# Performance work log

Measured on AMD Instinct MI355X. Metric: run time of the kernel, lower is better.

The kernel has to match this reference:

```python
import jax, jax.numpy as jnp
import numpy as np

EPS = 1e-07
INF = 100000.0
BIG = 1e8  # sentinel cost for priors outside all gt boxes/centers (filtered out in torch)
CENTER_RADIUS = 2.5
CANDIDATE_TOPK = 10
IOU_WEIGHT = 3.0
CLS_WEIGHT = 1.0
IMG = 1280.0


def setup_inputs() -> dict:
    key = jax.random.key(0)
    ks = jax.random.split(key, 9)
    N, G, C = 33600, 128, 80
    cx = jax.random.uniform(ks[0], (N,), minval=0.0, maxval=IMG)
    cy = jax.random.uniform(ks[1], (N,), minval=0.0, maxval=IMG)
    strides = jax.random.uniform(ks[2], (N, 2), minval=8.0, maxval=32.0)
    priors = jnp.stack([cx, cy, strides[:, 0], strides[:, 1]], axis=1)  # [N,4] cx,cy,sw,sh
    dc = jax.random.uniform(ks[3], (N, 2), minval=0.0, maxval=IMG)
    dwh = jax.random.uniform(ks[4], (N, 2), minval=4.0, maxval=200.0)
    decoded_bboxes = jnp.concatenate([dc - dwh / 2, dc + dwh / 2], axis=1)  # [N,4] tlbr
    gc = jax.random.uniform(ks[5], (G, 2), minval=0.0, maxval=IMG)
    gwh = jax.random.uniform(ks[6], (G, 2), minval=20.0, maxval=400.0)
    gt_bboxes = jnp.concatenate([gc - gwh / 2, gc + gwh / 2], axis=1)  # [G,4] tlbr
    pred_scores = jax.random.uniform(ks[7], (N, C), minval=1e-4, maxval=1.0 - 1e-4)
    gt_labels = jax.random.randint(ks[8], (G,), 0, C)
    return {
        'pred_scores': pred_scores,
        'priors': priors,
        'decoded_bboxes': decoded_bboxes,
        'gt_bboxes': gt_bboxes,
        'gt_labels': gt_labels,
    }


def _pairwise_iou(a, b):
    # a: [N,4] tlbr, b: [G,4] tlbr -> [N,G]
    tl = jnp.maximum(a[:, None, :2], b[None, :, :2])
    br = jnp.minimum(a[:, None, 2:], b[None, :, 2:])
    wh = jnp.clip(br - tl, 0.0)
    inter = wh[..., 0] * wh[..., 1]
    area_a = jnp.prod(jnp.clip(a[:, 2:] - a[:, :2], 0.0), axis=-1)
    area_b = jnp.prod(jnp.clip(b[:, 2:] - b[:, :2], 0.0), axis=-1)
    union = area_a[:, None] + area_b[None, :] - inter
    return inter / jnp.maximum(union, EPS)


def _forward(pred_scores, priors, decoded_bboxes, gt_bboxes, gt_labels):
    N = decoded_bboxes.shape[0]
    G = gt_bboxes.shape[0]
    px, py = priors[:, 0:1], priors[:, 1:2]          # [N,1]
    sx, sy = priors[:, 2:3], priors[:, 3:4]
    # in-gt-box mask [N,G]
    l_ = px - gt_bboxes[None, :, 0]
    t_ = py - gt_bboxes[None, :, 1]
    r_ = gt_bboxes[None, :, 2] - px
    b_ = gt_bboxes[None, :, 3] - py
    is_in_gts = jnp.minimum(jnp.minimum(l_, t_), jnp.minimum(r_, b_)) > 0
    # in-center mask [N,G]
    gcx = (gt_bboxes[:, 0] + gt_bboxes[:, 2]) / 2.0
    gcy = (gt_bboxes[:, 1] + gt_bboxes[:, 3]) / 2.0
    cl_ = px - (gcx[None, :] - CENTER_RADIUS * sx)
    ct_ = py - (gcy[None, :] - CENTER_RADIUS * sy)
    cr_ = (gcx[None, :] + CENTER_RADIUS * sx) - px
    cb_ = (gcy[None, :] + CENTER_RADIUS * sy) - py
    is_in_cts = jnp.minimum(jnp.minimum(cl_, ct_), jnp.minimum(cr_, cb_)) > 0
    valid = jnp.any(is_in_gts | is_in_cts, axis=1)           # [N]
    in_box_and_center = is_in_gts & is_in_cts                # [N,G]

    ious = _pairwise_iou(decoded_bboxes, gt_bboxes)          # [N,G]
    ious = jnp.where(valid[:, None], ious, 0.0)              # invalid priors excluded
    iou_cost = -jnp.log(ious + EPS)

    # BCE(pred, one_hot(label)).sum(-1) without materializing [N,G,C]:
    # = -log p[label] + log1p(-p[label]) - sum_c log1p(-p_c)  (logs clamped at -100 like torch)
    L = jnp.clip(jnp.log(pred_scores), -100.0)               # [N,C]
    L1 = jnp.clip(jnp.log1p(-pred_scores), -100.0)           # [N,C]
    gl = gt_labels.astype(jnp.int32)
    cls_cost = -(L[:, gl] - L1[:, gl]) - jnp.sum(L1, axis=1, keepdims=True)  # [N,G]

    cost = cls_cost * CLS_WEIGHT + iou_cost * IOU_WEIGHT + (~in_box_and_center) * INF
    cost = jnp.where(valid[:, None], cost, BIG)

    K = min(CANDIDATE_TOPK, N)
    topk_ious, _ = jax.lax.top_k(ious.T, K)                  # [G,K]
    dynamic_ks = jnp.clip(topk_ious.sum(1).astype(jnp.int32), 1, None)  # [G], <= K
    # per-GT: K smallest costs (ascending), keep first dynamic_k of them
    _, pos_idx = jax.lax.top_k(-cost.T, K)                   # [G,K] prior indices
    sel = (jnp.arange(K)[None, :] < dynamic_ks[:, None]).astype(cost.dtype)
    matching = jnp.zeros((N, G), cost.dtype).at[pos_idx, jnp.arange(G)[:, None]].add(sel)

    # resolve priors matched to >1 gt by min-cost gt
    multi = matching.sum(1) > 1
    argmin = jnp.argmin(cost, axis=1)
    matching = jnp.where(multi[:, None], jax.nn.one_hot(argmin, G, dtype=cost.dtype), matching)

    fg = matching.sum(1) > 0
    matched_gt = jnp.argmax(matching, axis=1)
    matched_iou = jnp.sum(matching * ious, axis=1)

    assigned_gt_inds = jnp.where(fg, matched_gt, 0)
    assigned_labels = jnp.where(fg, 1, -1)
    assigned_gt_iou = jnp.where(fg, matched_iou, -INF)
    return assigned_gt_inds, assigned_labels, assigned_gt_iou


def reference(pred_scores, priors, decoded_bboxes, gt_bboxes, gt_labels):
    return _forward(pred_scores, priors, decoded_bboxes, gt_bboxes, gt_labels)
```

## Files before the change

### kernel.cpp

```cpp
#include <hip/hip_runtime.h>
#include <math.h>
#include <limits.h>

#pragma clang fp contract(off)

#define TPB 256
#define ATPB 64
#define KTOP 10
#define ISPLIT 64
#define GSPLIT 8
#define GCAP 4096
#define CHUNKCAP 4224
#define MAXG 512
#define MAXMULTI 4096

typedef unsigned int u32;
typedef unsigned long long u64;
typedef unsigned char u8;

__device__ __forceinline__ float f_iou(float ax0, float ay0, float ax1, float ay1,
                                       float bx0, float by0, float bx1, float by1) {
  float tlx = fmaxf(ax0, bx0);
  float tly = fmaxf(ay0, by0);
  float brx = fminf(ax1, bx1);
  float bry = fminf(ay1, by1);
  float w = fmaxf(brx - tlx, 0.0f);
  float h = fmaxf(bry - tly, 0.0f);
  float inter = w * h;
  float aa = fmaxf(ax1 - ax0, 0.0f) * fmaxf(ay1 - ay0, 0.0f);
  float ab = fmaxf(bx1 - bx0, 0.0f) * fmaxf(by1 - by0, 0.0f);
  float uni = aa + ab - inter;
  return inter / fmaxf(uni, 1e-7f);
}

__device__ __forceinline__ float f_dv(float p) {
  float L  = fmaxf(logf(p), -100.0f);
  float L1 = fmaxf(log1pf(-p), -100.0f);
  return -(L - L1);
}

__device__ __forceinline__ float f_cost(float iou_masked, float dv, float sumL1v,
                                        float px, float py, float sx, float sy,
                                        float bx0, float by0, float bx1, float by1,
                                        int vld) {
  if (!vld) return 100000000.0f;
  float cls = dv - sumL1v;
  float l_ = px - bx0, t_ = py - by0, r_ = bx1 - px, b_ = by1 - py;
  bool ing = fminf(fminf(l_, t_), fminf(r_, b_)) > 0.0f;
  float gcx = (bx0 + bx1) * 0.5f;
  float gcy = (by0 + by1) * 0.5f;
  float cl = px - (gcx - 2.5f * sx);
  float ct = py - (gcy - 2.5f * sy);
  float cr = (gcx + 2.5f * sx) - px;
  float cb = (gcy + 2.5f * sy) - py;
  bool inc = fminf(fminf(cl, ct), fminf(cr, cb)) > 0.0f;
  float icost = -logf(iou_masked + 1e-7f);
  return (cls * 1.0f + icost * 3.0f) + ((ing && inc) ? 0.0f : 100000.0f);
}

__global__ __launch_bounds__(TPB) void k_fallback(float* out, int Nout) {
  int n = blockIdx.x * blockDim.x + threadIdx.x;
  if (n >= Nout) return;
  out[n] = 0.0f;
  out[Nout + n] = -1.0f;
  out[2 * Nout + n] = -70000.0f;
}

__global__ __launch_bounds__(TPB) void k_phase1(
    const float* pred, const float* priors, const float* gtb,
    float* sumL1, u32* packed, u8* validArr,
    int* gateCnt, int* gateList, int* flags,
    int N, int G, int C, int sumBlocks)
{
  __shared__ int lbuf[CHUNKCAP];
  __shared__ int lcnt;
  __shared__ int gbase;

  if ((int)blockIdx.x < sumBlocks) {
    int t = blockIdx.x * TPB + threadIdx.x;
    int n = t >> 3;
    int j = t & 7;
    if (n >= N) return;
    const float* pr = pred + (size_t)n * C;
    int lim = C - (C % 8);
    float r = 0.0f;
    for (int i = j; i < lim; i += 8) r += fmaxf(log1pf(-pr[i]), -100.0f);
    r += __shfl_down(r, 1, 8);
    r += __shfl_down(r, 2, 8);
    r += __shfl_down(r, 4, 8);
    if (j == 0) {
      for (int i = lim; i < C; ++i) r += fmaxf(log1pf(-pr[i]), -100.0f);
      sumL1[n] = r;
      packed[n] = 0;
    }
    return;
  }

  int bid = blockIdx.x - sumBlocks;
  int g = bid / GSPLIT;
  int s = bid % GSPLIT;
  int chunk = (N + GSPLIT - 1) / GSPLIT;
  int start = s * chunk;
  int end = start + chunk; if (end > N) end = N;
  int lane = threadIdx.x & 63;

  if (threadIdx.x == 0) lcnt = 0;
  __syncthreads();

  float x0 = gtb[g * 4 + 0], y0 = gtb[g * 4 + 1];
  float x1 = gtb[g * 4 + 2], y1 = gtb[g * 4 + 3];
  float gcx = (x0 + x1) * 0.5f, gcy = (y0 + y1) * 0.5f;
  const float4* pri4 = reinterpret_cast<const float4*>(priors);

  for (int nb = start; nb < end; nb += TPB) {
    int n = nb + threadIdx.x;
    bool gated = false;
    if (n < end) {
      float4 pv = pri4[n];
      float px = pv.x, py = pv.y, sx = pv.z, sy = pv.w;
      float l_ = px - x0, t_ = py - y0, r_ = x1 - px, b_ = y1 - py;
      bool ing = fminf(fminf(l_, t_), fminf(r_, b_)) > 0.0f;
      float cl = px - (gcx - 2.5f * sx), ct = py - (gcy - 2.5f * sy);
      float cr = (gcx + 2.5f * sx) - px, cb = (gcy + 2.5f * sy) - py;
      bool inc = fminf(fminf(cl, ct), fminf(cr, cb)) > 0.0f;
      if (ing || inc) validArr[n] = 1;
      gated = ing && inc;
    }
    u64 mask = __ballot(gated);
    int wcnt = __popcll(mask);
    int wbase = 0;
    if (lane == 0 && wcnt > 0) wbase = atomicAdd(&lcnt, wcnt);
    wbase = __shfl(wbase, 0);
    if (gated) {
      int p = __popcll(mask & ((1ull << lane) - 1ull));
      lbuf[wbase + p] = n;
    }
  }
  __syncthreads();
  int total = lcnt;
  if (threadIdx.x == 0 && total > 0) gbase = atomicAdd(&gateCnt[g], total);
  __syncthreads();
  if (total > 0) {
    int base = gbase;
    int* gl = gateList + (size_t)g * GCAP;
    for (int i = threadIdx.x; i < total; i += TPB) {
      int slot = base + i;
      if (slot < GCAP) gl[slot] = lbuf[i];
      else flags[g] = 1;
    }
  }
}

__global__ __launch_bounds__(ATPB) void k_iou_part(
    const float* dec, const u8* validArr, const float* gtb,
    float* iouV, int N, int G)
{
  int bid = blockIdx.x;
  int g = bid / ISPLIT;
  int s = bid % ISPLIT;
  int chunk = (N + ISPLIT - 1) / ISPLIT;
  int start = s * chunk;
  int end = start + chunk; if (end > N) end = N;
  int tid = threadIdx.x;
  float bx0 = gtb[g * 4 + 0];
  float by0 = gtb[g * 4 + 1];
  float bx1 = gtb[g * 4 + 2];
  float by1 = gtb[g * 4 + 3];

  float iv[KTOP];
#pragma unroll
  for (int j = 0; j < KTOP; ++j) iv[j] = 0.0f;

  const float4* dec4 = reinterpret_cast<const float4*>(dec);
  for (int n = start + tid; n < end; n += ATPB) {
    float4 dvb = dec4[n];
    float iou = f_iou(dvb.x, dvb.y, dvb.z, dvb.w, bx0, by0, bx1, by1);
    if (!validArr[n]) iou = 0.0f;
    if (iou > iv[KTOP - 1]) {
      float cu = iou;
#pragma unroll
      for (int j = 0; j < KTOP; ++j) {
        if (cu > iv[j]) { float tv = iv[j]; iv[j] = cu; cu = tv; }
      }
    }
  }

#pragma unroll
  for (int r = 0; r < KTOP; ++r) {
    float v = iv[0]; int owner = tid;
#pragma unroll
    for (int off = 32; off > 0; off >>= 1) {
      float v2 = __shfl_down(v, off);
      int o2 = __shfl_down(owner, off);
      if (v2 > v || (v2 == v && o2 < owner)) { v = v2; owner = o2; }
    }
    float wv = __shfl(v, 0);
    int wo = __shfl(owner, 0);
    if (tid == 0) iouV[bid * KTOP + r] = wv;
    if (tid == wo) {
#pragma unroll
      for (int j = 0; j < KTOP - 1; ++j) iv[j] = iv[j + 1];
      iv[KTOP - 1] = 0.0f;
    }
  }
}

__global__ __launch_bounds__(ATPB) void k_merge(
    const float* iouV, const int* gateCnt, const int* gateList, const int* flags,
    const float* pred, const float* priors, const float* dec, const float* sumL1,
    const u8* validArr, const int* gtl, const float* gtb,
    u32* packed, int G, int N, int C)
{
  int g = blockIdx.x;
  int tid = threadIdx.x;
  int base = g * ISPLIT * KTOP;
  const int TOT = ISPLIT * KTOP;
  const int PER = TOT / ATPB;

  float il[PER];
#pragma unroll
  for (int k = 0; k < PER; ++k) il[k] = 0.0f;
#pragma unroll
  for (int k = 0; k < PER; ++k) {
    float v = iouV[base + tid + k * ATPB];
    if (v > il[PER - 1]) {
#pragma unroll
      for (int j = 0; j < PER; ++j) {
        if (v > il[j]) { float tv = il[j]; il[j] = v; v = tv; }
      }
    }
  }
  float rv[KTOP];
#pragma unroll
  for (int r = 0; r < KTOP; ++r) {
    float v = il[0]; int owner = tid;
#pragma unroll
    for (int off = 32; off > 0; off >>= 1) {
      float v2 = __shfl_down(v, off);
      int o2 = __shfl_down(owner, off);
      if (v2 > v || (v2 == v && o2 < owner)) { v = v2; owner = o2; }
    }
    float wv = __shfl(v, 0);
    int wo = __shfl(owner, 0);
    rv[r] = wv;
    if (tid == wo) {
#pragma unroll
      for (int j = 0; j < PER - 1; ++j) il[j] = il[j + 1];
      il[PER - 1] = 0.0f;
    }
  }
  float s8 = ((rv[0] + rv[1]) + (rv[2] + rv[3])) + ((rv[4] + rv[5]) + (rv[6] + rv[7]));
  s8 += rv[8];
  s8 += rv[9];
  int dk = (int)s8;
  if (dk < 1) dk = 1;
  if (dk > KTOP) dk = KTOP;

  float bx0 = gtb[g * 4 + 0];
  float by0 = gtb[g * 4 + 1];
  float bx1 = gtb[g * 4 + 2];
  float by1 = gtb[g * 4 + 3];
  int lab = gtl[g];
  if (lab < 0) lab = 0;
  if (lab >= C) lab = C - 1;

  float cv[KTOP]; int ci[KTOP];
#pragma unroll
  for (int j = 0; j < KTOP; ++j) { cv[j] = 1e30f; ci[j] = INT_MAX; }
  const float4* dec4 = reinterpret_cast<const float4*>(dec);

  int cnt = gateCnt[g];
  if (!flags[g] && cnt >= KTOP) {
    const int* gl = gateList + (size_t)g * GCAP;
    for (int i = tid; i < cnt; i += ATPB) {
      int n = gl[i];
      float4 dvb = dec4[n];
      float iou = f_iou(dvb.x, dvb.y, dvb.z, dvb.w, bx0, by0, bx1, by1);
      float dv = f_dv(pred[(size_t)n * C + lab]);
      float cls = dv - sumL1[n];
      float icost = -logf(iou + 1e-7f);
      float c = (cls * 1.0f + icost * 3.0f) + 0.0f;
      bool ins = (c < cv[KTOP - 1]) || (c == cv[KTOP - 1] && n < ci[KTOP - 1]);
      if (ins) {
        float cu = c; int cui = n;
#pragma unroll
        for (int j = 0; j < KTOP; ++j) {
          bool lt = (cu < cv[j]) || (cu == cv[j] && cui < ci[j]);
          if (lt) { float tv = cv[j]; int ti = ci[j]; cv[j] = cu; ci[j] = cui; cu = tv; cui = ti; }
        }
      }
    }
  } else {
    const float4* pri4 = reinterpret_cast<const float4*>(priors);
    for (int n = tid; n < N; n += ATPB) {
      float4 dvb = dec4[n];
      int vld = validArr[n];
      float iou = f_iou(dvb.x, dvb.y, dvb.z, dvb.w, bx0, by0, bx1, by1);
      if (!vld) iou = 0.0f;
      float dv = f_dv(pred[(size_t)n * C + lab]);
      float4 pv = pri4[n];
      float c = f_cost(iou, dv, sumL1[n], pv.x, pv.y, pv.z, pv.w, bx0, by0, bx1, by1, vld);
      bool ins = (c < cv[KTOP - 1]) || (c == cv[KTOP - 1] && n < ci[KTOP - 1]);
      if (ins) {
        float cu = c; int cui = n;
#pragma unroll
        for (int j = 0; j < KTOP; ++j) {
          bool lt = (cu < cv[j]) || (cu == cv[j] && cui < ci[j]);
          if (lt) { float tv = cv[j]; int ti = ci[j]; cv[j] = cu; ci[j] = cui; cu = tv; cui = ti; }
        }
      }
    }
  }

  for (int r = 0; r < KTOP; ++r) {
    float v = cv[0]; int idx = ci[0];
#pragma unroll
    for (int off = 32; off > 0; off >>= 1) {
      float v2 = __shfl_down(v, off);
      int i2 = __shfl_down(idx, off);
      if (v2 < v || (v2 == v && i2 < idx)) { v = v2; idx = i2; }
    }
    int wi = __shfl(idx, 0);
    if (r < dk && tid == 0 && wi >= 0 && wi < N) {
      atomicAdd(&packed[wi], (1u << 16) | (u32)g);
    }
    if (ci[0] == wi) {
#pragma unroll
      for (int j = 0; j < KTOP - 1; ++j) { cv[j] = cv[j + 1]; ci[j] = ci[j + 1]; }
      cv[KTOP - 1] = 1e30f; ci[KTOP - 1] = INT_MAX;
    }
    if (r + 1 >= dk) break;
  }
}

__global__ __launch_bounds__(TPB) void k_final(
    const float* dec, const float* gtb, const u8* validArr, const u32* packed,
    int* mlist, int* mcnt,
    float* out, int N, int G, int Nout)
{
  __shared__ float sg[MAXG * 4];
  for (int i = threadIdx.x; i < G * 4; i += blockDim.x) sg[i] = gtb[i];
  __syncthreads();
  int n = blockIdx.x * blockDim.x + threadIdx.x;
  if (n >= N || n >= Nout) return;
  u32 pk = packed[n];
  int cnt = (int)(pk >> 16);
  float o0 = 0.0f, o1 = -1.0f, o2 = -100000.0f;
  if (cnt > 1) {
    int idx = atomicAdd(mcnt, 1);
    if (idx < MAXMULTI) mlist[idx] = n;
  }
  if (cnt == 1) {
    int g = (int)(pk & 0xFFFFu);
    if (g < 0) g = 0;
    if (g >= G) g = G - 1;
    const float4 dv = reinterpret_cast<const float4*>(dec)[n];
    float x0 = sg[g * 4 + 0], y0 = sg[g * 4 + 1], x1 = sg[g * 4 + 2], y1 = sg[g * 4 + 3];
    float iou = f_iou(dv.x, dv.y, dv.z, dv.w, x0, y0, x1, y1);
    if (!validArr[n]) iou = 0.0f;
    o0 = (float)g; o1 = 1.0f; o2 = iou;
  }
  out[n]            = o0;
  out[Nout + n]     = o1;
  out[2 * Nout + n] = o2;
}

#define MTPB 128
__global__ __launch_bounds__(MTPB) void k_multi(
    const float* pred, const float* priors, const float* dec,
    const float* gtb, const int* gtl, const float* sumL1, const u8* validArr,
    const int* mlist, const int* mcnt,
    float* out, int N, int G, int C, int Nout)
{
  __shared__ float rv[MTPB];
  __shared__ int   rg[MTPB];
  int tid = threadIdx.x;
  int total = *mcnt;
  if (total > MAXMULTI) total = MAXMULTI;
  for (int w = blockIdx.x; w < total; w += gridDim.x) {
    int n = mlist[w];
    const float4 dvb = reinterpret_cast<const float4*>(dec)[n];
    const float4 pv  = reinterpret_cast<const float4*>(priors)[n];
    float s1 = sumL1[n];
    int vld = validArr[n];
    float best = 1e30f; int bg = INT_MAX;
    for (int gg = tid; gg < G; gg += MTPB) {
      float x0 = gtb[gg * 4 + 0], y0 = gtb[gg * 4 + 1];
      float x1 = gtb[gg * 4 + 2], y1 = gtb[gg * 4 + 3];
      float iou = f_iou(dvb.x, dvb.y, dvb.z, dvb.w, x0, y0, x1, y1);
      if (!vld) iou = 0.0f;
      int lb = gtl[gg];
      if (lb < 0) lb = 0;
      if (lb >= C) lb = C - 1;
      float dv = f_dv(pred[(size_t)n * C + lb]);
      float c = f_cost(iou, dv, s1, pv.x, pv.y, pv.z, pv.w, x0, y0, x1, y1, vld);
      if (c < best || (c == best && gg < bg)) { best = c; bg = gg; }
    }
    rv[tid] = best; rg[tid] = bg;
    __syncthreads();
    for (int st = MTPB / 2; st > 0; st >>= 1) {
      if (tid < st) {
        float v2 = rv[tid + st]; int g2 = rg[tid + st];
        float v1 = rv[tid];      int g1 = rg[tid];
        if (v2 < v1 || (v2 == v1 && g2 < g1)) { rv[tid] = v2; rg[tid] = g2; }
      }
      __syncthreads();
    }
    if (tid == 0) {
      int g = rg[0];
      if (g < 0 || g >= G) g = 0;
      float x0 = gtb[g * 4 + 0], y0 = gtb[g * 4 + 1];
      float x1 = gtb[g * 4 + 2], y1 = gtb[g * 4 + 3];
      float iou = f_iou(dvb.x, dvb.y, dvb.z, dvb.w, x0, y0, x1, y1);
      if (!vld) iou = 0.0f;
      out[n]            = (float)g;
      out[Nout + n]     = 1.0f;
      out[2 * Nout + n] = iou;
    }
    __syncthreads();
  }
}

extern "C" void kernel_launch(void* const* d_in, const int* in_sizes, int n_in,
                              void* d_out, int out_size, void* d_ws, size_t ws_size,
                              hipStream_t stream) {
  const float* pred   = (const float*)d_in[0];
  const float* priors = (const float*)d_in[1];
  const float* dec    = (const float*)d_in[2];
  const float* gtb    = (const float*)d_in[3];
  const int*   gtl    = (const int*)d_in[4];
  int N = in_sizes[2] / 4;
  int G = in_sizes[3] / 4;
  if (G > MAXG) G = MAXG;
  int C = in_sizes[0] / N;
  int Nout = out_size / 3;
  float* out = (float*)d_out;

  size_t offPacked = 0;
  size_t offSum    = offPacked + (size_t)N * 4;
  size_t offZero   = (offSum + (size_t)N * 4 + 15) & ~(size_t)15;
  size_t offFlags  = offZero + (size_t)G * 4;
  size_t offMcnt   = offFlags + (size_t)G * 4;
  size_t offValid  = (offMcnt + 4 + 15) & ~(size_t)15;
  size_t offMlist  = (offValid + (size_t)N + 15) & ~(size_t)15;
  size_t offGlist  = (offMlist + (size_t)MAXMULTI * 4 + 15) & ~(size_t)15;
  size_t offIouV   = offGlist + (size_t)G * GCAP * 4;
  size_t need      = offIouV + (size_t)G * ISPLIT * KTOP * 4;

  dim3 b(TPB);
  int nblk = (N + TPB - 1) / TPB;
  int oblk = (Nout + TPB - 1) / TPB;
  if (ws_size < need || d_ws == nullptr) {
    k_fallback<<<oblk, b, 0, stream>>>(out, Nout);
    return;
  }
  char* wsb = (char*)d_ws;
  u32* packed   = (u32*)(wsb + offPacked);
  float* sumL1  = (float*)(wsb + offSum);
  int* gateCnt  = (int*)(wsb + offZero);
  int* flags    = (int*)(wsb + offFlags);
  int* mcnt     = (int*)(wsb + offMcnt);
  u8* validArr  = (u8*)(wsb + offValid);
  int* mlist    = (int*)(wsb + offMlist);
  int* gateList = (int*)(wsb + offGlist);
  float* iouV   = (float*)(wsb + offIouV);

  hipMemsetAsync(wsb + offZero, 0, offValid + (size_t)N - offZero, stream);

  int sumBlocks = ((N * 8) + TPB - 1) / TPB;
  int gateBlocks = G * GSPLIT;
  k_phase1<<<sumBlocks + gateBlocks, b, 0, stream>>>(
      pred, priors, gtb, sumL1, packed, validArr, gateCnt, gateList, flags,
      N, G, C, sumBlocks);
  k_iou_part<<<G * ISPLIT, dim3(ATPB), 0, stream>>>(dec, validArr, gtb, iouV, N, G);
  k_merge<<<G, dim3(ATPB), 0, stream>>>(iouV, gateCnt, gateList, flags,
                                        pred, priors, dec, sumL1, validArr, gtl, gtb,
                                        packed, G, N, C);
  k_final<<<nblk, b, 0, stream>>>(dec, gtb, validArr, packed, mlist, mcnt, out, N, G, Nout);
  k_multi<<<256, dim3(MTPB), 0, stream>>>(pred, priors, dec, gtb, gtl, sumL1, validArr,
                                          mlist, mcnt, out, N, G, C, Nout);
}
```

Before: 127.1 us.

## Fuse all assignment stages into one cooperative persistent kernel with grid syncs

Replaces the memset and five separate kernel launches with a single cooperative kernel. The stages (log-sum and gating, per-chunk IoU top-k, per-GT merge and cost top-k, final write, multi-match resolution) are separated by grid.sync, and each wave now handles one unit instead of each 64-thread block. The intent is to remove launch overhead and inter-kernel gaps and to use wave-level shuffles instead of shared-memory reductions in the multi stage. The cost is grid-wide barriers and a grid sized by occupancy (up to 1024 blocks), which may underuse the GPU in the heavier stages. The gating stage also gains in-loop flushing of the shared buffer.

```diff
diff --git a/kernel.cpp b/kernel.cpp
--- a/kernel.cpp
+++ b/kernel.cpp
@@ -1,18 +1,20 @@
 #include <hip/hip_runtime.h>
+#include <hip/hip_cooperative_groups.h>
 #include <math.h>
 #include <limits.h>
 
 #pragma clang fp contract(off)
 
 #define TPB 256
-#define ATPB 64
+#define NWAVE 4
 #define KTOP 10
 #define ISPLIT 64
 #define GSPLIT 8
 #define GCAP 4096
-#define CHUNKCAP 4224
-#define MAXG 512
+#define CHUNKCAP 4480
 #define MAXMULTI 4096
+
+namespace cg = cooperative_groups;
 
 typedef unsigned int u32;
 typedef unsigned long long u64;
@@ -58,333 +60,328 @@
   return (cls * 1.0f + icost * 3.0f) + ((ing && inc) ? 0.0f : 100000.0f);
 }
 
-__global__ __launch_bounds__(TPB) void k_fallback(float* out, int Nout) {
+__global__ __launch_bounds__(TPB) void k_fb(float* out, int Nout, float val) {
   int n = blockIdx.x * blockDim.x + threadIdx.x;
   if (n >= Nout) return;
   out[n] = 0.0f;
   out[Nout + n] = -1.0f;
-  out[2 * Nout + n] = -70000.0f;
-}
-
-__global__ __launch_bounds__(TPB) void k_phase1(
-    const float* pred, const float* priors, const float* gtb,
+  out[2 * Nout + n] = val;
+}
+
+__global__ __launch_bounds__(TPB) void k_all(
+    const float* pred, const float* priors, const float* dec,
+    const float* gtb, const int* gtl,
     float* sumL1, u32* packed, u8* validArr,
     int* gateCnt, int* gateList, int* flags,
-    int N, int G, int C, int sumBlocks)
+    float* iouV, int* mlist, int* mcnt,
+    float* out, int N, int G, int C, int Nout)
 {
+  cg::grid_group grid = cg::this_grid();
   __shared__ int lbuf[CHUNKCAP];
   __shared__ int lcnt;
   __shared__ int gbase;
-
-  if ((int)blockIdx.x < sumBlocks) {
-    int t = blockIdx.x * TPB + threadIdx.x;
-    int n = t >> 3;
-    int j = t & 7;
-    if (n >= N) return;
-    const float* pr = pred + (size_t)n * C;
-    int lim = C - (C % 8);
-    float r = 0.0f;
-    for (int i = j; i < lim; i += 8) r += fmaxf(log1pf(-pr[i]), -100.0f);
-    r += __shfl_down(r, 1, 8);
-    r += __shfl_down(r, 2, 8);
-    r += __shfl_down(r, 4, 8);
-    if (j == 0) {
-      for (int i = lim; i < C; ++i) r += fmaxf(log1pf(-pr[i]), -100.0f);
-      sumL1[n] = r;
-      packed[n] = 0;
-    }
-    return;
-  }
-
-  int bid = blockIdx.x - sumBlocks;
-  int g = bid / GSPLIT;
-  int s = bid % GSPLIT;
-  int chunk = (N + GSPLIT - 1) / GSPLIT;
-  int start = s * chunk;
-  int end = start + chunk; if (end > N) end = N;
-  int lane = threadIdx.x & 63;
-
-  if (threadIdx.x == 0) lcnt = 0;
-  __syncthreads();
-
-  float x0 = gtb[g * 4 + 0], y0 = gtb[g * 4 + 1];
-  float x1 = gtb[g * 4 + 2], y1 = gtb[g * 4 + 3];
-  float gcx = (x0 + x1) * 0.5f, gcy = (y0 + y1) * 0.5f;
+  const int tid = threadIdx.x;
+  const int lane = tid & 63;
+  const int wid = tid >> 6;
+  const int nblk = gridDim.x;
+  const float4* dec4 = reinterpret_cast<const float4*>(dec);
   const float4* pri4 = reinterpret_cast<const float4*>(priors);
 
-  for (int nb = start; nb < end; nb += TPB) {
-    int n = nb + threadIdx.x;
-    bool gated = false;
-    if (n < end) {
-      float4 pv = pri4[n];
-      float px = pv.x, py = pv.y, sx = pv.z, sy = pv.w;
-      float l_ = px - x0, t_ = py - y0, r_ = x1 - px, b_ = y1 - py;
-      bool ing = fminf(fminf(l_, t_), fminf(r_, b_)) > 0.0f;
-      float cl = px - (gcx - 2.5f * sx), ct = py - (gcy - 2.5f * sy);
-      float cr = (gcx + 2.5f * sx) - px, cb = (gcy + 2.5f * sy) - py;
-      bool inc = fminf(fminf(cl, ct), fminf(cr, cb)) > 0.0f;
-      if (ing || inc) validArr[n] = 1;
-      gated = ing && inc;
-    }
-    u64 mask = __ballot(gated);
-    int wcnt = __popcll(mask);
-    int wbase = 0;
-    if (lane == 0 && wcnt > 0) wbase = atomicAdd(&lcnt, wcnt);
-    wbase = __shfl(wbase, 0);
-    if (gated) {
-      int p = __popcll(mask & ((1ull << lane) - 1ull));
-      lbuf[wbase + p] = n;
-    }
-  }
-  __syncthreads();
-  int total = lcnt;
-  if (threadIdx.x == 0 && total > 0) gbase = atomicAdd(&gateCnt[g], total);
-  __syncthreads();
-  if (total > 0) {
-    int base = gbase;
-    int* gl = gateList + (size_t)g * GCAP;
-    for (int i = threadIdx.x; i < total; i += TPB) {
-      int slot = base + i;
-      if (slot < GCAP) gl[slot] = lbuf[i];
-      else flags[g] = 1;
-    }
-  }
-}
-
-__global__ __launch_bounds__(ATPB) void k_iou_part(
-    const float* dec, const u8* validArr, const float* gtb,
-    float* iouV, int N, int G)
-{
-  int bid = blockIdx.x;
-  int g = bid / ISPLIT;
-  int s = bid % ISPLIT;
-  int chunk = (N + ISPLIT - 1) / ISPLIT;
-  int start = s * chunk;
-  int end = start + chunk; if (end > N) end = N;
-  int tid = threadIdx.x;
-  float bx0 = gtb[g * 4 + 0];
-  float by0 = gtb[g * 4 + 1];
-  float bx1 = gtb[g * 4 + 2];
-  float by1 = gtb[g * 4 + 3];
-
-  float iv[KTOP];
-#pragma unroll
-  for (int j = 0; j < KTOP; ++j) iv[j] = 0.0f;
-
-  const float4* dec4 = reinterpret_cast<const float4*>(dec);
-  for (int n = start + tid; n < end; n += ATPB) {
-    float4 dvb = dec4[n];
-    float iou = f_iou(dvb.x, dvb.y, dvb.z, dvb.w, bx0, by0, bx1, by1);
-    if (!validArr[n]) iou = 0.0f;
-    if (iou > iv[KTOP - 1]) {
-      float cu = iou;
-#pragma unroll
-      for (int j = 0; j < KTOP; ++j) {
-        if (cu > iv[j]) { float tv = iv[j]; iv[j] = cu; cu = tv; }
-      }
-    }
-  }
-
-#pragma unroll
-  for (int r = 0; r < KTOP; ++r) {
-    float v = iv[0]; int owner = tid;
-#pragma unroll
-    for (int off = 32; off > 0; off >>= 1) {
-      float v2 = __shfl_down(v, off);
-      int o2 = __shfl_down(owner, off);
-      if (v2 > v || (v2 == v && o2 < owner)) { v = v2; owner = o2; }
-    }
-    float wv = __shfl(v, 0);
-    int wo = __shfl(owner, 0);
-    if (tid == 0) iouV[bid * KTOP + r] = wv;
-    if (tid == wo) {
-#pragma unroll
-      for (int j = 0; j < KTOP - 1; ++j) iv[j] = iv[j + 1];
-      iv[KTOP - 1] = 0.0f;
-    }
-  }
-}
-
-__global__ __launch_bounds__(ATPB) void k_merge(
-    const float* iouV, const int* gateCnt, const int* gateList, const int* flags,
-    const float* pred, const float* priors, const float* dec, const float* sumL1,
-    const u8* validArr, const int* gtl, const float* gtb,
-    u32* packed, int G, int N, int C)
-{
-  int g = blockIdx.x;
-  int tid = threadIdx.x;
-  int base = g * ISPLIT * KTOP;
-  const int TOT = ISPLIT * KTOP;
-  const int PER = TOT / ATPB;
-
-  float il[PER];
-#pragma unroll
-  for (int k = 0; k < PER; ++k) il[k] = 0.0f;
-#pragma unroll
-  for (int k = 0; k < PER; ++k) {
-    float v = iouV[base + tid + k * ATPB];
-    if (v > il[PER - 1]) {
-#pragma unroll
-      for (int j = 0; j < PER; ++j) {
-        if (v > il[j]) { float tv = il[j]; il[j] = v; v = tv; }
-      }
-    }
-  }
-  float rv[KTOP];
-#pragma unroll
-  for (int r = 0; r < KTOP; ++r) {
-    float v = il[0]; int owner = tid;
-#pragma unroll
-    for (int off = 32; off > 0; off >>= 1) {
-      float v2 = __shfl_down(v, off);
-      int o2 = __shfl_down(owner, off);
-      if (v2 > v || (v2 == v && o2 < owner)) { v = v2; owner = o2; }
-    }
-    float wv = __shfl(v, 0);
-    int wo = __shfl(owner, 0);
-    rv[r] = wv;
-    if (tid == wo) {
-#pragma unroll
-      for (int j = 0; j < PER - 1; ++j) il[j] = il[j + 1];
-      il[PER - 1] = 0.0f;
-    }
-  }
-  float s8 = ((rv[0] + rv[1]) + (rv[2] + rv[3])) + ((rv[4] + rv[5]) + (rv[6] + rv[7]));
-  s8 += rv[8];
-  s8 += rv[9];
-  int dk = (int)s8;
-  if (dk < 1) dk = 1;
-  if (dk > KTOP) dk = KTOP;
-
-  float bx0 = gtb[g * 4 + 0];
-  float by0 = gtb[g * 4 + 1];
-  float bx1 = gtb[g * 4 + 2];
-  float by1 = gtb[g * 4 + 3];
-  int lab = gtl[g];
-  if (lab < 0) lab = 0;
-  if (lab >= C) lab = C - 1;
-
-  float cv[KTOP]; int ci[KTOP];
-#pragma unroll
-  for (int j = 0; j < KTOP; ++j) { cv[j] = 1e30f; ci[j] = INT_MAX; }
-  const float4* dec4 = reinterpret_cast<const float4*>(dec);
-
-  int cnt = gateCnt[g];
-  if (!flags[g] && cnt >= KTOP) {
-    const int* gl = gateList + (size_t)g * GCAP;
-    for (int i = tid; i < cnt; i += ATPB) {
-      int n = gl[i];
+  for (int i = blockIdx.x * TPB + tid; i < N; i += nblk * TPB) {
+    packed[i] = 0;
+    validArr[i] = 0;
+  }
+  for (int i = blockIdx.x * TPB + tid; i < G; i += nblk * TPB) {
+    gateCnt[i] = 0;
+    flags[i] = 0;
+  }
+  if (blockIdx.x == 0 && tid == 0) *mcnt = 0;
+  grid.sync();
+
+  int sumUnits = (N * 8 + TPB - 1) / TPB;
+  int gateUnits = G * GSPLIT;
+  int chunkG = (N + GSPLIT - 1) / GSPLIT;
+  for (int u = blockIdx.x; u < sumUnits + gateUnits; u += nblk) {
+    if (u < sumUnits) {
+      int t = u * TPB + tid;
+      int n = t >> 3, j = t & 7;
+      if (n < N) {
+        const float* pr = pred + (size_t)n * C;
+        int lim = C - (C % 8);
+        float r = 0.0f;
+        for (int i = j; i < lim; i += 8) r += fmaxf(log1pf(-pr[i]), -100.0f);
+        r += __shfl_down(r, 1, 8);
+        r += __shfl_down(r, 2, 8);
+        r += __shfl_down(r, 4, 8);
+        if (j == 0) {
+          for (int i = lim; i < C; ++i) r += fmaxf(log1pf(-pr[i]), -100.0f);
+          sumL1[n] = r;
+        }
+      }
+    } else {
+      int bidg = u - sumUnits;
+      int g = bidg / GSPLIT, s = bidg % GSPLIT;
+      int start = s * chunkG;
+      int end = start + chunkG; if (end > N) end = N;
+      float x0 = gtb[g * 4 + 0], y0 = gtb[g * 4 + 1];
+      float x1 = gtb[g * 4 + 2], y1 = gtb[g * 4 + 3];
+      float gcx = (x0 + x1) * 0.5f, gcy = (y0 + y1) * 0.5f;
+      int* gl = gateList + (size_t)g * GCAP;
+      if (tid == 0) lcnt = 0;
+      __syncthreads();
+      for (int nb = start; nb < end; nb += TPB) {
+        __syncthreads();
+        if (lcnt + TPB > CHUNKCAP) {
+          int total = lcnt;
+          if (tid == 0) gbase = atomicAdd(&gateCnt[g], total);
+          __syncthreads();
+          int base = gbase;
+          for (int i = tid; i < total; i += TPB) {
+            int slot = base + i;
+            if (slot < GCAP) gl[slot] = lbuf[i];
+            else flags[g] = 1;
+          }
+          __syncthreads();
+          if (tid == 0) lcnt = 0;
+          __syncthreads();
+        }
+        int n = nb + tid;
+        bool gated = false;
+        if (n < end) {
+          float4 pv = pri4[n];
+          float px = pv.x, py = pv.y, sx = pv.z, sy = pv.w;
+          float l_ = px - x0, t_ = py - y0, r_ = x1 - px, b_ = y1 - py;
+          bool ing = fminf(fminf(l_, t_), fminf(r_, b_)) > 0.0f;
+          float cl = px - (gcx - 2.5f * sx), ct = py - (gcy - 2.5f * sy);
+          float cr = (gcx + 2.5f * sx) - px, cb = (gcy + 2.5f * sy) - py;
+          bool inc = fminf(fminf(cl, ct), fminf(cr, cb)) > 0.0f;
+          if (ing || inc) validArr[n] = 1;
+          gated = ing && inc;
+        }
+        u64 mask = __ballot(gated);
+        int wcnt = __popcll(mask);
+        int wbase = 0;
+        if (lane == 0 && wcnt > 0) wbase = atomicAdd(&lcnt, wcnt);
+        wbase = __shfl(wbase, 0);
+        if (gated) {
+          int p = __popcll(mask & ((1ull << lane) - 1ull));
+          lbuf[wbase + p] = n;
+        }
+      }
+      __syncthreads();
+      int total = lcnt;
+      if (tid == 0 && total > 0) gbase = atomicAdd(&gateCnt[g], total);
+      __syncthreads();
+      if (total > 0) {
+        int base = gbase;
+        for (int i = tid; i < total; i += TPB) {
+          int slot = base + i;
+          if (slot < GCAP) gl[slot] = lbuf[i];
+          else flags[g] = 1;
+        }
+      }
+      __syncthreads();
+    }
+  }
+  grid.sync();
+
+  int chunkI = (N + ISPLIT - 1) / ISPLIT;
+  for (int u = blockIdx.x * NWAVE + wid; u < G * ISPLIT; u += nblk * NWAVE) {
+    int g = u / ISPLIT, s = u % ISPLIT;
+    int start = s * chunkI;
+    int end = start + chunkI; if (end > N) end = N;
+    float bx0 = gtb[g * 4 + 0], by0 = gtb[g * 4 + 1];
+    float bx1 = gtb[g * 4 + 2], by1 = gtb[g * 4 + 3];
+    float iv[KTOP];
+#pragma unroll
+    for (int j = 0; j < KTOP; ++j) iv[j] = 0.0f;
+    for (int n = start + lane; n < end; n += 64) {
       float4 dvb = dec4[n];
       float iou = f_iou(dvb.x, dvb.y, dvb.z, dvb.w, bx0, by0, bx1, by1);
-      float dv = f_dv(pred[(size_t)n * C + lab]);
-      float cls = dv - sumL1[n];
-      float icost = -logf(iou + 1e-7f);
-      float c = (cls * 1.0f + icost * 3.0f) + 0.0f;
-      bool ins = (c < cv[KTOP - 1]) || (c == cv[KTOP - 1] && n < ci[KTOP - 1]);
-      if (ins) {
-        float cu = c; int cui = n;
+      if (!validArr[n]) iou = 0.0f;
+      if (iou > iv[KTOP - 1]) {
+        float cu = iou;
 #pragma unroll
         for (int j = 0; j < KTOP; ++j) {
-          bool lt = (cu < cv[j]) || (cu == cv[j] && cui < ci[j]);
-          if (lt) { float tv = cv[j]; int ti = ci[j]; cv[j] = cu; ci[j] = cui; cu = tv; cui = ti; }
-        }
-      }
-    }
-  } else {
-    const float4* pri4 = reinterpret_cast<const float4*>(priors);
-    for (int n = tid; n < N; n += ATPB) {
-      float4 dvb = dec4[n];
-      int vld = validArr[n];
-      float iou = f_iou(dvb.x, dvb.y, dvb.z, dvb.w, bx0, by0, bx1, by1);
-      if (!vld) iou = 0.0f;
-      float dv = f_dv(pred[(size_t)n * C + lab]);
-      float4 pv = pri4[n];
-      float c = f_cost(iou, dv, sumL1[n], pv.x, pv.y, pv.z, pv.w, bx0, by0, bx1, by1, vld);
-      bool ins = (c < cv[KTOP - 1]) || (c == cv[KTOP - 1] && n < ci[KTOP - 1]);
-      if (ins) {
-        float cu = c; int cui = n;
-#pragma unroll
-        for (int j = 0; j < KTOP; ++j) {
-          bool lt = (cu < cv[j]) || (cu == cv[j] && cui < ci[j]);
-          if (lt) { float tv = cv[j]; int ti = ci[j]; cv[j] = cu; ci[j] = cui; cu = tv; cui = ti; }
-        }
-      }
-    }
-  }
-
-  for (int r = 0; r < KTOP; ++r) {
-    float v = cv[0]; int idx = ci[0];
-#pragma unroll
-    for (int off = 32; off > 0; off >>= 1) {
-      float v2 = __shfl_down(v, off);
-      int i2 = __shfl_down(idx, off);
-      if (v2 < v || (v2 == v && i2 < idx)) { v = v2; idx = i2; }
-    }
-    int wi = __shfl(idx, 0);
-    if (r < dk && tid == 0 && wi >= 0 && wi < N) {
-      atomicAdd(&packed[wi], (1u << 16) | (u32)g);
-    }
-    if (ci[0] == wi) {
-#pragma unroll
-      for (int j = 0; j < KTOP - 1; ++j) { cv[j] = cv[j + 1]; ci[j] = ci[j + 1]; }
-      cv[KTOP - 1] = 1e30f; ci[KTOP - 1] = INT_MAX;
-    }
-    if (r + 1 >= dk) break;
-  }
-}
-
-__global__ __launch_bounds__(TPB) void k_final(
-    const float* dec, const float* gtb, const u8* validArr, const u32* packed,
-    int* mlist, int* mcnt,
-    float* out, int N, int G, int Nout)
-{
-  __shared__ float sg[MAXG * 4];
-  for (int i = threadIdx.x; i < G * 4; i += blockDim.x) sg[i] = gtb[i];
-  __syncthreads();
-  int n = blockIdx.x * blockDim.x + threadIdx.x;
-  if (n >= N || n >= Nout) return;
-  u32 pk = packed[n];
-  int cnt = (int)(pk >> 16);
-  float o0 = 0.0f, o1 = -1.0f, o2 = -100000.0f;
-  if (cnt > 1) {
-    int idx = atomicAdd(mcnt, 1);
-    if (idx < MAXMULTI) mlist[idx] = n;
-  }
-  if (cnt == 1) {
-    int g = (int)(pk & 0xFFFFu);
-    if (g < 0) g = 0;
-    if (g >= G) g = G - 1;
-    const float4 dv = reinterpret_cast<const float4*>(dec)[n];
-    float x0 = sg[g * 4 + 0], y0 = sg[g * 4 + 1], x1 = sg[g * 4 + 2], y1 = sg[g * 4 + 3];
-    float iou = f_iou(dv.x, dv.y, dv.z, dv.w, x0, y0, x1, y1);
-    if (!validArr[n]) iou = 0.0f;
-    o0 = (float)g; o1 = 1.0f; o2 = iou;
-  }
-  out[n]            = o0;
-  out[Nout + n]     = o1;
-  out[2 * Nout + n] = o2;
-}
-
-#define MTPB 128
-__global__ __launch_bounds__(MTPB) void k_multi(
-    const float* pred, const float* priors, const float* dec,
-    const float* gtb, const int* gtl, const float* sumL1, const u8* validArr,
-    const int* mlist, const int* mcnt,
-    float* out, int N, int G, int C, int Nout)
-{
-  __shared__ float rv[MTPB];
-  __shared__ int   rg[MTPB];
-  int tid = threadIdx.x;
+          if (cu > iv[j]) { float tv = iv[j]; iv[j] = cu; cu = tv; }
+        }
+      }
+    }
+#pragma unroll
+    for (int r = 0; r < KTOP; ++r) {
+      float v = iv[0]; int owner = lane;
+#pragma unroll
+      for (int off = 32; off > 0; off >>= 1) {
+        float v2 = __shfl_down(v, off);
+        int o2 = __shfl_down(owner, off);
+        if (v2 > v || (v2 == v && o2 < owner)) { v = v2; owner = o2; }
+      }
+      float wv = __shfl(v, 0);
+      int wo = __shfl(owner, 0);
+      if (lane == 0) iouV[u * KTOP + r] = wv;
+      if (lane == wo) {
+#pragma unroll
+        for (int j = 0; j < KTOP - 1; ++j) iv[j] = iv[j + 1];
+        iv[KTOP - 1] = 0.0f;
+      }
+    }
+  }
+  grid.sync();
+
+  for (int g = blockIdx.x * NWAVE + wid; g < G; g += nblk * NWAVE) {
+    int base = g * ISPLIT * KTOP;
+    const int TOT = ISPLIT * KTOP;
+    const int PER = TOT / 64;
+    float il[PER];
+#pragma unroll
+    for (int k = 0; k < PER; ++k) il[k] = 0.0f;
+#pragma unroll
+    for (int k = 0; k < PER; ++k) {
+      float v = iouV[base + lane + k * 64];
+      if (v > il[PER - 1]) {
+#pragma unroll
+        for (int j = 0; j < PER; ++j) {
+          if (v > il[j]) { float tv = il[j]; il[j] = v; v = tv; }
+        }
+      }
+    }
+    float rv[KTOP];
+#pragma unroll
+    for (int r = 0; r < KTOP; ++r) {
+      float v = il[0]; int owner = lane;
+#pragma unroll
+      for (int off = 32; off > 0; off >>= 1) {
+        float v2 = __shfl_down(v, off);
+        int o2 = __shfl_down(owner, off);
+        if (v2 > v || (v2 == v && o2 < owner)) { v = v2; owner = o2; }
+      }
+      float wv = __shfl(v, 0);
+      int wo = __shfl(owner, 0);
+      rv[r] = wv;
+      if (lane == wo) {
+#pragma unroll
+        for (int j = 0; j < PER - 1; ++j) il[j] = il[j + 1];
+        il[PER - 1] = 0.0f;
+      }
+    }
+    float s8 = ((rv[0] + rv[1]) + (rv[2] + rv[3])) + ((rv[4] + rv[5]) + (rv[6] + rv[7]));
+    s8 += rv[8];
+    s8 += rv[9];
+    int dk = (int)s8;
+    if (dk < 1) dk = 1;
+    if (dk > KTOP) dk = KTOP;
+
+    float bx0 = gtb[g * 4 + 0], by0 = gtb[g * 4 + 1];
+    float bx1 = gtb[g * 4 + 2], by1 = gtb[g * 4 + 3];
+    int lab = gtl[g];
+    if (lab < 0) lab = 0;
+    if (lab >= C) lab = C - 1;
+
+    float cv[KTOP]; int ci[KTOP];
+#pragma unroll
+    for (int j = 0; j < KTOP; ++j) { cv[j] = 1e30f; ci[j] = INT_MAX; }
+
+    int cnt = gateCnt[g];
+    if (!flags[g] && cnt >= KTOP) {
+      const int* gl = gateList + (size_t)g * GCAP;
+      for (int i = lane; i < cnt; i += 64) {
+        int n = gl[i];
+        float4 dvb = dec4[n];
+        float iou = f_iou(dvb.x, dvb.y, dvb.z, dvb.w, bx0, by0, bx1, by1);
+        float dv = f_dv(pred[(size_t)n * C + lab]);
+        float cls = dv - sumL1[n];
+        float icost = -logf(iou + 1e-7f);
+        float c = (cls * 1.0f + icost * 3.0f) + 0.0f;
+        bool ins = (c < cv[KTOP - 1]) || (c == cv[KTOP - 1] && n < ci[KTOP - 1]);
+        if (ins) {
+          float cu = c; int cui = n;
+#pragma unroll
+          for (int j = 0; j < KTOP; ++j) {
+            bool lt = (cu < cv[j]) || (cu == cv[j] && cui < ci[j]);
+            if (lt) { float tv = cv[j]; int ti = ci[j]; cv[j] = cu; ci[j] = cui; cu = tv; cui = ti; }
+          }
+        }
+      }
+    } else {
+      for (int n = lane; n < N; n += 64) {
+        float4 dvb = dec4[n];
+        int vld = validArr[n];
+        float iou = f_iou(dvb.x, dvb.y, dvb.z, dvb.w, bx0, by0, bx1, by1);
+        if (!vld) iou = 0.0f;
+        float dv = f_dv(pred[(size_t)n * C + lab]);
+        float4 pv = pri4[n];
+        float c = f_cost(iou, dv, sumL1[n], pv.x, pv.y, pv.z, pv.w,
+                         bx0, by0, bx1, by1, vld);
+        bool ins = (c < cv[KTOP - 1]) || (c == cv[KTOP - 1] && n < ci[KTOP - 1]);
+        if (ins) {
+          float cu = c; int cui = n;
+#pragma unroll
+          for (int j = 0; j < KTOP; ++j) {
+            bool lt = (cu < cv[j]) || (cu == cv[j] && cui < ci[j]);
+            if (lt) { float tv = cv[j]; int ti = ci[j]; cv[j] = cu; ci[j] = cui; cu = tv; cui = ti; }
+          }
+        }
+      }
+    }
+
+    for (int r = 0; r < KTOP; ++r) {
+      float v = cv[0]; int idx = ci[0];
+#pragma unroll
+      for (int off = 32; off > 0; off >>= 1) {
+        float v2 = __shfl_down(v, off);
+        int i2 = __shfl_down(idx, off);
+        if (v2 < v || (v2 == v && i2 < idx)) { v = v2; idx = i2; }
+      }
+      int wi = __shfl(idx, 0);
+      if (r < dk && lane == 0 && wi >= 0 && wi < N) {
+        atomicAdd(&packed[wi], (1u << 16) | (u32)g);
+      }
+      if (ci[0] == wi) {
+#pragma unroll
+        for (int j = 0; j < KTOP - 1; ++j) { cv[j] = cv[j + 1]; ci[j] = ci[j + 1]; }
+        cv[KTOP - 1] = 1e30f; ci[KTOP - 1] = INT_MAX;
+      }
+      if (r + 1 >= dk) break;
+    }
+  }
+  grid.sync();
+
+  for (int n = blockIdx.x * TPB + tid; n < N; n += nblk * TPB) {
+    if (n >= Nout) break;
+    u32 pk = packed[n];
+    int cnt = (int)(pk >> 16);
+    float o0 = 0.0f, o1 = -1.0f, o2 = -100000.0f;
+    if (cnt > 1) {
+      int idx = atomicAdd(mcnt, 1);
+      if (idx < MAXMULTI) mlist[idx] = n;
+    }
+    if (cnt == 1) {
+      int g = (int)(pk & 0xFFFFu);
+      if (g < 0) g = 0;
+      if (g >= G) g = G - 1;
+      float4 dv = dec4[n];
+      float x0 = gtb[g * 4 + 0], y0 = gtb[g * 4 + 1];
+      float x1 = gtb[g * 4 + 2], y1 = gtb[g * 4 + 3];
+      float iou = f_iou(dv.x, dv.y, dv.z, dv.w, x0, y0, x1, y1);
+      if (!validArr[n]) iou = 0.0f;
+      o0 = (float)g; o1 = 1.0f; o2 = iou;
+    }
+    out[n]            = o0;
+    out[Nout + n]     = o1;
+    out[2 * Nout + n] = o2;
+  }
+  grid.sync();
+
   int total = *mcnt;
   if (total > MAXMULTI) total = MAXMULTI;
-  for (int w = blockIdx.x; w < total; w += gridDim.x) {
+  for (int w = blockIdx.x * NWAVE + wid; w < total; w += nblk * NWAVE) {
     int n = mlist[w];
-    const float4 dvb = reinterpret_cast<const float4*>(dec)[n];
-    const float4 pv  = reinterpret_cast<const float4*>(priors)[n];
+    float4 dvb = dec4[n];
+    float4 pv = pri4[n];
     float s1 = sumL1[n];
     int vld = validArr[n];
     float best = 1e30f; int bg = INT_MAX;
-    for (int gg = tid; gg < G; gg += MTPB) {
+    for (int gg = lane; gg < G; gg += 64) {
       float x0 = gtb[gg * 4 + 0], y0 = gtb[gg * 4 + 1];
       float x1 = gtb[gg * 4 + 2], y1 = gtb[gg * 4 + 3];
       float iou = f_iou(dvb.x, dvb.y, dvb.z, dvb.w, x0, y0, x1, y1);
@@ -396,18 +393,14 @@
       float c = f_cost(iou, dv, s1, pv.x, pv.y, pv.z, pv.w, x0, y0, x1, y1, vld);
       if (c < best || (c == best && gg < bg)) { best = c; bg = gg; }
     }
-    rv[tid] = best; rg[tid] = bg;
-    __syncthreads();
-    for (int st = MTPB / 2; st > 0; st >>= 1) {
-      if (tid < st) {
-        float v2 = rv[tid + st]; int g2 = rg[tid + st];
-        float v1 = rv[tid];      int g1 = rg[tid];
-        if (v2 < v1 || (v2 == v1 && g2 < g1)) { rv[tid] = v2; rg[tid] = g2; }
-      }
-      __syncthreads();
-    }
-    if (tid == 0) {
-      int g = rg[0];
+#pragma unroll
+    for (int off = 32; off > 0; off >>= 1) {
+      float v2 = __shfl_down(best, off);
+      int g2 = __shfl_down(bg, off);
+      if (v2 < best || (v2 == best && g2 < bg)) { best = v2; bg = g2; }
+    }
+    if (lane == 0 && n < Nout) {
+      int g = bg;
       if (g < 0 || g >= G) g = 0;
       float x0 = gtb[g * 4 + 0], y0 = gtb[g * 4 + 1];
       float x1 = gtb[g * 4 + 2], y1 = gtb[g * 4 + 3];
@@ -417,7 +410,6 @@
       out[Nout + n]     = 1.0f;
       out[2 * Nout + n] = iou;
     }
-    __syncthreads();
   }
 }
 
@@ -431,52 +423,56 @@
   const int*   gtl    = (const int*)d_in[4];
   int N = in_sizes[2] / 4;
   int G = in_sizes[3] / 4;
-  if (G > MAXG) G = MAXG;
   int C = in_sizes[0] / N;
   int Nout = out_size / 3;
   float* out = (float*)d_out;
 
   size_t offPacked = 0;
   size_t offSum    = offPacked + (size_t)N * 4;
-  size_t offZero   = (offSum + (size_t)N * 4 + 15) & ~(size_t)15;
-  size_t offFlags  = offZero + (size_t)G * 4;
+  size_t offValid  = offSum + (size_t)N * 4;
+  size_t offGate   = (offValid + (size_t)N + 15) & ~(size_t)15;
+  size_t offFlags  = offGate + (size_t)G * 4;
   size_t offMcnt   = offFlags + (size_t)G * 4;
-  size_t offValid  = (offMcnt + 4 + 15) & ~(size_t)15;
-  size_t offMlist  = (offValid + (size_t)N + 15) & ~(size_t)15;
+  size_t offMlist  = (offMcnt + 4 + 15) & ~(size_t)15;
   size_t offGlist  = (offMlist + (size_t)MAXMULTI * 4 + 15) & ~(size_t)15;
   size_t offIouV   = offGlist + (size_t)G * GCAP * 4;
   size_t need      = offIouV + (size_t)G * ISPLIT * KTOP * 4;
 
   dim3 b(TPB);
-  int nblk = (N + TPB - 1) / TPB;
   int oblk = (Nout + TPB - 1) / TPB;
   if (ws_size < need || d_ws == nullptr) {
-    k_fallback<<<oblk, b, 0, stream>>>(out, Nout);
+    k_fb<<<oblk, b, 0, stream>>>(out, Nout, -70000.0f);
     return;
   }
   char* wsb = (char*)d_ws;
   u32* packed   = (u32*)(wsb + offPacked);
   float* sumL1  = (float*)(wsb + offSum);
-  int* gateCnt  = (int*)(wsb + offZero);
+  u8* validArr  = (u8*)(wsb + offValid);
+  int* gateCnt  = (int*)(wsb + offGate);
   int* flags    = (int*)(wsb + offFlags);
   int* mcnt     = (int*)(wsb + offMcnt);
-  u8* validArr  = (u8*)(wsb + offValid);
   int* mlist    = (int*)(wsb + offMlist);
   int* gateList = (int*)(wsb + offGlist);
   float* iouV   = (float*)(wsb + offIouV);
 
-  hipMemsetAsync(wsb + offZero, 0, offValid + (size_t)N - offZero, stream);
-
-  int sumBlocks = ((N * 8) + TPB - 1) / TPB;
-  int gateBlocks = G * GSPLIT;
-  k_phase1<<<sumBlocks + gateBlocks, b, 0, stream>>>(
-      pred, priors, gtb, sumL1, packed, validArr, gateCnt, gateList, flags,
-      N, G, C, sumBlocks);
-  k_iou_part<<<G * ISPLIT, dim3(ATPB), 0, stream>>>(dec, validArr, gtb, iouV, N, G);
-  k_merge<<<G, dim3(ATPB), 0, stream>>>(iouV, gateCnt, gateList, flags,
-                                        pred, priors, dec, sumL1, validArr, gtl, gtb,
-                                        packed, G, N, C);
-  k_final<<<nblk, b, 0, stream>>>(dec, gtb, validArr, packed, mlist, mcnt, out, N, G, Nout);
-  k_multi<<<256, dim3(MTPB), 0, stream>>>(pred, priors, dec, gtb, gtl, sumL1, validArr,
-                                          mlist, mcnt, out, N, G, C, Nout);
-}
+  int maxBlocksPerCU = 0;
+  hipError_t oe = hipOccupancyMaxActiveBlocksPerMultiprocessor(
+      &maxBlocksPerCU, (const void*)k_all, TPB, 0);
+  if (oe != hipSuccess || maxBlocksPerCU < 1) maxBlocksPerCU = 1;
+  int grid = maxBlocksPerCU * 256;
+  if (grid > 1024) grid = 1024;
+  if (grid < 64) grid = 64;
+
+  void* args[] = {
+    (void*)&pred, (void*)&priors, (void*)&dec, (void*)&gtb, (void*)&gtl,
+    (void*)&sumL1, (void*)&packed, (void*)&validArr,
+    (void*)&gateCnt, (void*)&gateList, (void*)&flags,
+    (void*)&iouV, (void*)&mlist, (void*)&mcnt,
+    (void*)&out, (void*)&N, (void*)&G, (void*)&C, (void*)&Nout
+  };
+  hipError_t err = hipLaunchCooperativeKernel(
+      (const void*)k_all, dim3(grid), dim3(TPB), args, 0, stream);
+  if (err != hipSuccess) {
+    k_fb<<<oblk, b, 0, stream>>>(out, Nout, -80000.0f);
+  }
+}
```

New measurement: 423.3 us. +232.9%, slower.
